# Optimization experiments

Measured on AMD Instinct MI355X. Metric: run time of the kernel, lower is better.

Reference implementation:

```python
import jax, jax.numpy as jnp
from jax import lax
import numpy as np

B, T = 32, 64
E, H, V = 512, 512, 10000


def setup_inputs() -> dict:
    key = jax.random.key(0)
    ks = jax.random.split(key, 9)
    s = 0.02
    return {
        "features": jax.random.normal(ks[0], (B, E), dtype=jnp.float32),
        "captions": jax.random.randint(ks[1], (B, T), 0, V, dtype=jnp.int64),
        "forward_approach": 0,
        "embed_table": jax.random.normal(ks[2], (V, E), dtype=jnp.float32) * s,
        "W_ih": jax.random.normal(ks[3], (4 * H, E), dtype=jnp.float32) * s,
        "W_hh": jax.random.normal(ks[4], (4 * H, H), dtype=jnp.float32) * s,
        "b_ih": jax.random.normal(ks[5], (4 * H,), dtype=jnp.float32) * s,
        "b_hh": jax.random.normal(ks[6], (4 * H,), dtype=jnp.float32) * s,
        "fc_W": jax.random.normal(ks[7], (V, H), dtype=jnp.float32) * s,
        "fc_b": jax.random.normal(ks[8], (V,), dtype=jnp.float32) * s,
    }


def reference(features, captions, forward_approach, embed_table,
              W_ih, W_hh, b_ih, b_hh, fc_W, fc_b):
    # features: [B, E]; captions: [B, T] int
    batch = features.shape[0]
    seq_len = captions.shape[1]
    hidden = W_hh.shape[1]

    # Input at step 0 is `features`; at step t>0 it is embed(captions[:, t-1]).
    emb = embed_table[captions[:, : seq_len - 1]]            # [B, T-1, E]
    xs = jnp.concatenate([features[None], jnp.transpose(emb, (1, 0, 2))],
                         axis=0)                              # [T, B, E]

    def step(carry, x):
        h, c = carry
        # PyTorch LSTMCell gate order: i, f, g, o
        gates = x @ W_ih.T + b_ih + h @ W_hh.T + b_hh         # [B, 4H]
        i, f, g, o = jnp.split(gates, 4, axis=-1)
        i = jax.nn.sigmoid(i)
        f = jax.nn.sigmoid(f)
        g = jnp.tanh(g)
        o = jax.nn.sigmoid(o)
        c = f * c + i * g
        h = o * jnp.tanh(c)
        return (h, c), h

    h0 = jnp.zeros((batch, hidden), dtype=features.dtype)
    c0 = jnp.zeros((batch, hidden), dtype=features.dtype)
    _, hs = lax.scan(step, (h0, c0), xs)                      # [T, B, H]

    logits = jnp.einsum('tbh,vh->tbv', hs, fc_W) + fc_b       # [T, B, V]
    return jnp.transpose(logits, (1, 0, 2))                   # [B, T, V]
```

## Files before the change

### kernel.cpp

```cpp
#include <hip/hip_runtime.h>
#include <hip/hip_bf16.h>

#define B_ 32
#define T_ 64
#define E_ 512
#define H_ 512
#define V_ 10000
#define G4 2048

#define NLSTM 64
#define NFC   157
#define NTOT  (NLSTM + NFC)

using bf16x8 = __attribute__((ext_vector_type(8))) short;
using f32x4  = __attribute__((ext_vector_type(4))) float;

__device__ inline f32x4 mfma16(bf16x8 a, bf16x8 b, f32x4 c) {
  return __builtin_amdgcn_mfma_f32_16x16x32_bf16(a, b, c, 0, 0, 0);
}

__device__ inline short f2bf(float x) {
  unsigned u = __builtin_bit_cast(unsigned, x);
  u = (u + 0x7fffu + ((u >> 16) & 1u)) >> 16;
  return (short)u;
}

__device__ inline float fsigm(float x) {
  return __builtin_amdgcn_rcpf(1.f + __builtin_amdgcn_exp2f(-1.442695040888963f * x));
}
__device__ inline float ftanh(float x) {
  return 1.f - 2.f * __builtin_amdgcn_rcpf(1.f + __builtin_amdgcn_exp2f(2.885390081777927f * x));
}

__device__ inline bf16x8 lds_ld16B(const short* base, int row, int col) {
  int byte = (row << 10) + (col << 1);
  byte ^= (row & 7) << 4;
  return *(const bf16x8*)((const char*)base + byte);
}

__device__ inline bf16x8 cast8(const float* src) {
  float4 f0 = *(const float4*)src;
  float4 f1 = *(const float4*)(src + 4);
  bf16x8 v;
  v[0] = f2bf(f0.x); v[1] = f2bf(f0.y); v[2] = f2bf(f0.z); v[3] = f2bf(f0.w);
  v[4] = f2bf(f1.x); v[5] = f2bf(f1.y); v[6] = f2bf(f1.z); v[7] = f2bf(f1.w);
  return v;
}


#define NW (G4 * E_)
#define NA (NW + G4)
#define NB (NA + T_ * B_ * E_)

__global__ void prep_kernel(const float* __restrict__ W_ih,
                            const float* __restrict__ b_ih, const float* __restrict__ b_hh,
                            const float* __restrict__ features, const int* __restrict__ captions,
                            const float* __restrict__ embed,
                            short* __restrict__ wih_bf, float* __restrict__ bsum,
                            short* __restrict__ xs) {
  int i = blockIdx.x * blockDim.x + threadIdx.x;
  int stride = gridDim.x * blockDim.x;
  for (; i < NB; i += stride) {
    if (i < NW) {
      wih_bf[i] = f2bf(W_ih[i]);
    } else if (i < NA) {
      int j = i - NW;
      bsum[j] = b_ih[j] + b_hh[j];
    } else {
      int j = i - NA;
      int t = j / (B_ * E_);
      int r = j - t * (B_ * E_);
      int b = r >> 9;
      int e = r & 511;
      float v;
      if (t == 0) v = features[b * E_ + e];
      else        v = embed[captions[b * T_ + (t - 1)] * E_ + e];
      xs[j] = f2bf(v);
    }
  }
}


__global__ __launch_bounds__(256) void gemm_gx_kernel(const short* __restrict__ A,
                                                      const short* __restrict__ W,
                                                      const float* __restrict__ bias,
                                                      float* __restrict__ C) {
  const int lane = threadIdx.x & 63;
  const int wv   = threadIdx.x >> 6;
  const int m0 = blockIdx.y * 64 + (wv >> 1) * 32;
  const int n0 = blockIdx.x * 64 + (wv & 1) * 32;
  const int lr = lane & 15;
  const int ko = (lane >> 4) << 3;
  f32x4 acc[2][2] = {};
  const short* Ap = A + (m0 + lr) * 512 + ko;
  const short* Wp = W + (n0 + lr) * 512 + ko;
#pragma unroll
  for (int k = 0; k < 512; k += 32) {
    bf16x8 a0 = *(const bf16x8*)(Ap + k);
    bf16x8 a1 = *(const bf16x8*)(Ap + 16 * 512 + k);
    bf16x8 b0 = *(const bf16x8*)(Wp + k);
    bf16x8 b1 = *(const bf16x8*)(Wp + 16 * 512 + k);
    acc[0][0] = mfma16(a0, b0, acc[0][0]);
    acc[0][1] = mfma16(a0, b1, acc[0][1]);
    acc[1][0] = mfma16(a1, b0, acc[1][0]);
    acc[1][1] = mfma16(a1, b1, acc[1][1]);
  }
  const int cr = (lane >> 4) * 4, cc = lane & 15;
#pragma unroll
  for (int mi = 0; mi < 2; ++mi)
#pragma unroll
    for (int ni = 0; ni < 2; ++ni)
#pragma unroll
      for (int j = 0; j < 4; ++j) {
        int row = m0 + mi * 16 + cr + j;
        int col = n0 + ni * 16 + cc;
        int tt = row >> 5, bb = row & 31;
        int g  = col >> 9, hc = col & 511;
        C[(size_t)((tt * 4 + g) * 32 + bb) * 512 + hc] = acc[mi][ni][j] + bias[col];
      }
}


__global__ __launch_bounds__(256) void fused_kernel(const float* __restrict__ WhhF,
                                                    const float* __restrict__ Gx,
                                                    short* __restrict__ hs,
                                                    int* __restrict__ flags,
                                                    const float* __restrict__ fcWF,
                                                    const float* __restrict__ fcbias,
                                                    float* __restrict__ out) {
  __shared__ short Wlds[64 * 512];
  __shared__ int tready;
  const int tid = threadIdx.x;
  int* const cnt = flags + 256;

  if (blockIdx.x < NLSTM) {
    const int blk  = blockIdx.x;
    const int bg   = blk >> 5;
    const int slot = blk & 31;
    const int hc0  = slot * 16;
    int* const gflags = flags + bg * 32;

    for (int i = tid * 8; i < 64 * 512; i += 256 * 8) {
      int gc = i >> 9;
      int k  = i & 511;
      int g  = gc >> 4, c = gc & 15;
      bf16x8 v = cast8(WhhF + (size_t)(g * 512 + hc0 + c) * 512 + k);
      int byte = (i * 2) ^ ((gc & 7) << 4);
      *(bf16x8*)((char*)Wlds + byte) = v;
    }
    __syncthreads();
    if (tid >= 64) return;

    const int lane = tid;
    const int lr  = lane & 15;
    const int ko  = (lane >> 4) << 3;
    const int cr  = (lane >> 4) << 2;
    const int cc  = lane & 15;
    const int bat = bg * 16 + cc;
    const int hrow = bg * 16 + lr;

    const float* gbase = Gx + (size_t)bat * 512 + hc0 + cr;
    float4 gx0 = *(const float4*)(gbase + 0 * 32 * 512);
    float4 gx1 = *(const float4*)(gbase + 1 * 32 * 512);
    float4 gx2 = *(const float4*)(gbase + 2 * 32 * 512);
    float4 gx3 = *(const float4*)(gbase + 3 * 32 * 512);

    float cst[4] = {0.f, 0.f, 0.f, 0.f};

    for (int t = 0; t < T_; ++t) {
      f32x4 a0 = {}, a1 = {}, a2 = {}, a3 = {};
      if (t > 0) {
        const int* fp = gflags + (lane & 31);
        for (;;) {
          int fl = __hip_atomic_load(fp, __ATOMIC_RELAXED, __HIP_MEMORY_SCOPE_AGENT);
          if (__all(fl >= t)) break;
        }
        asm volatile("" ::: "memory");
        const short* Ap = hs + (size_t)(t - 1) * (B_ * H_) + hrow * 512 + ko;
#pragma unroll
        for (int kk = 0; kk < 512; kk += 32) {
          bf16x8 hb = *(const bf16x8*)(Ap + kk);
          bf16x8 w0 = lds_ld16B(Wlds,      lr, kk + ko);
          bf16x8 w1 = lds_ld16B(Wlds, 16 + lr, kk + ko);
          bf16x8 w2 = lds_ld16B(Wlds, 32 + lr, kk + ko);
          bf16x8 w3 = lds_ld16B(Wlds, 48 + lr, kk + ko);
          a0 = mfma16(w0, hb, a0);
          a1 = mfma16(w1, hb, a1);
          a2 = mfma16(w2, hb, a2);
          a3 = mfma16(w3, hb, a3);
        }
      }
      unsigned long long hpack = 0;
#pragma unroll
      for (int j = 0; j < 4; ++j) {
        float iv = fsigm(a0[j] + ((const float*)&gx0)[j]);
        float fv = fsigm(a1[j] + ((const float*)&gx1)[j]);
        float gv = ftanh(a2[j] + ((const float*)&gx2)[j]);
        float ov = fsigm(a3[j] + ((const float*)&gx3)[j]);
        float cv = fv * cst[j] + iv * gv;
        cst[j] = cv;
        float hv = ov * ftanh(cv);
        hpack |= (unsigned long long)(unsigned short)f2bf(hv) << (16 * j);
      }
      __hip_atomic_store(
          (unsigned long long*)(hs + (size_t)t * (B_ * H_) + bat * 512 + hc0 + cr),
          hpack, __ATOMIC_RELAXED, __HIP_MEMORY_SCOPE_AGENT);
      asm volatile("s_waitcnt vmcnt(0)" ::: "memory");
      if (lane == 0) {
        if (t < T_ - 1)
          __hip_atomic_store(gflags + slot, t + 1, __ATOMIC_RELAXED,
                             __HIP_MEMORY_SCOPE_AGENT);
        __hip_atomic_fetch_add(cnt + t, 1, __ATOMIC_RELAXED,
                               __HIP_MEMORY_SCOPE_AGENT);
      }
      if (t < T_ - 1) {
        const float* g0 = gbase + (size_t)(t + 1) * 128 * 512;
        gx0 = *(const float4*)(g0 + 0 * 32 * 512);
        gx1 = *(const float4*)(g0 + 1 * 32 * 512);
        gx2 = *(const float4*)(g0 + 2 * 32 * 512);
        gx3 = *(const float4*)(g0 + 3 * 32 * 512);
      }
    }
  } else {
    const int fblk = blockIdx.x - NLSTM;
    const int n0   = fblk * 64;
    const int lane = tid & 63;
    const int wv   = tid >> 6;
    const int lr   = lane & 15;
    const int ko   = (lane >> 4) << 3;

    if (tid == 0)
      __hip_atomic_store(&tready, 0, __ATOMIC_RELAXED, __HIP_MEMORY_SCOPE_WORKGROUP);

    for (int i = tid * 8; i < 64 * 512; i += 256 * 8) {
      int gc = i >> 9;
      int k  = i & 511;
      int nr = n0 + gc; if (nr >= V_) nr = V_ - 1;
      bf16x8 v = cast8(fcWF + (size_t)nr * 512 + k);
      int byte = (i * 2) ^ ((gc & 7) << 4);
      *(bf16x8*)((char*)Wlds + byte) = v;
    }
    __syncthreads();

    const int cr = (lane >> 4) * 4, cc = lane & 15;
    const int colw = n0 + wv * 16 + cc;
    const bool wok = colw < V_;
    const float bias = wok ? fcbias[colw] : 0.f;

    for (int t = 0; t < T_; ++t) {
      if (wv == 0) {
        for (;;) {
          int c = __hip_atomic_load(cnt + t, __ATOMIC_RELAXED,
                                    __HIP_MEMORY_SCOPE_AGENT);
          if (c >= NLSTM) break;
          __builtin_amdgcn_s_sleep(32);
        }
        __hip_atomic_store(&tready, t + 1, __ATOMIC_RELAXED,
                           __HIP_MEMORY_SCOPE_WORKGROUP);
      } else {
        while (__hip_atomic_load(&tready, __ATOMIC_RELAXED,
                                 __HIP_MEMORY_SCOPE_WORKGROUP) < t + 1)
          __builtin_amdgcn_s_sleep(2);
      }
      asm volatile("" ::: "memory");
      const short* Ap = hs + (size_t)t * (B_ * H_) + lr * 512 + ko;
      f32x4 acc0 = {}, acc1 = {};
#pragma unroll
      for (int k = 0; k < 512; k += 32) {
        bf16x8 a0 = *(const bf16x8*)(Ap + k);
        bf16x8 a1 = *(const bf16x8*)(Ap + 16 * 512 + k);
        bf16x8 b  = lds_ld16B(Wlds, wv * 16 + lr, k + ko);
        acc0 = mfma16(a0, b, acc0);
        acc1 = mfma16(a1, b, acc1);
      }
      if (wok) {
#pragma unroll
        for (int j = 0; j < 4; ++j) {
          out[(size_t)(cr + j) * (T_ * V_) + t * V_ + colw]      = acc0[j] + bias;
          out[(size_t)(16 + cr + j) * (T_ * V_) + t * V_ + colw] = acc1[j] + bias;
        }
      }
    }
  }
}


extern "C" void kernel_launch(void* const* d_in, const int* in_sizes, int n_in,
                              void* d_out, int out_size, void* d_ws, size_t ws_size,
                              hipStream_t stream) {
  const float* features = (const float*)d_in[0];
  const int*   captions = (const int*)d_in[1];
  const float* embed    = (const float*)d_in[3];
  const float* W_ih     = (const float*)d_in[4];
  const float* W_hh     = (const float*)d_in[5];
  const float* b_ih     = (const float*)d_in[6];
  const float* b_hh     = (const float*)d_in[7];
  const float* fc_W     = (const float*)d_in[8];
  const float* fc_b     = (const float*)d_in[9];
  float* out = (float*)d_out;

  char* ws = (char*)d_ws;
  size_t off = 0;
  auto alloc = [&](size_t bytes) -> void* {
    off = (off + 255) & ~(size_t)255;
    void* p = ws + off;
    off += bytes;
    return p;
  };
  int*      flags  = (int*)  alloc(4096);
  short*    wih_bf = (short*)alloc((size_t)G4 * E_ * 2);
  float*    bsum   = (float*)alloc((size_t)G4 * 4);
  float*    Gx     = (float*)alloc((size_t)T_ * B_ * G4 * 4);
  short*    xs     = (short*)alloc((size_t)T_ * B_ * E_ * 2);
  short*    hs     = (short*)alloc((size_t)T_ * B_ * H_ * 2);

  (void)hipMemsetAsync(flags, 0, 4096, stream);
  prep_kernel<<<1024, 256, 0, stream>>>(W_ih, b_ih, b_hh, features, captions,
                                        embed, wih_bf, bsum, xs);
  gemm_gx_kernel<<<dim3(32, 32), 256, 0, stream>>>(xs, wih_bf, bsum, Gx);
  fused_kernel<<<NTOT, 256, 0, stream>>>(W_hh, Gx, hs, flags, fc_W, fc_b, out);
}
```

Measured before the change: 308.3 us.

## Fuse input-projection GEMM into persistent LSTM blocks using LDS-resident W_ih slices

Removes the separate gemm_gx kernel and the Gx intermediate buffer. Each LSTM block now also holds its slice of W_ih (as bf16) in shared memory and computes x_t @ W_ih^T with MFMA inside the timestep loop, before waiting on the recurrence flags. This drops a kernel launch, the W_ih conversion pass, and the Gx write and read traffic. In exchange, LDS use per block doubles to 128KB, and the extra MFMA work runs inside the serial recurrence, though it can overlap with the flag wait.

```diff
diff --git a/kernel.cpp b/kernel.cpp
--- a/kernel.cpp
+++ b/kernel.cpp
@@ -48,24 +48,17 @@
 }
 
 
-#define NW (G4 * E_)
-#define NA (NW + G4)
-#define NB (NA + T_ * B_ * E_)
-
-__global__ void prep_kernel(const float* __restrict__ W_ih,
-                            const float* __restrict__ b_ih, const float* __restrict__ b_hh,
+__global__ void prep_kernel(const float* __restrict__ b_ih, const float* __restrict__ b_hh,
                             const float* __restrict__ features, const int* __restrict__ captions,
                             const float* __restrict__ embed,
-                            short* __restrict__ wih_bf, float* __restrict__ bsum,
-                            short* __restrict__ xs) {
+                            float* __restrict__ bsum, short* __restrict__ xs) {
   int i = blockIdx.x * blockDim.x + threadIdx.x;
   int stride = gridDim.x * blockDim.x;
+  const int NA = G4;
+  const int NB = NA + T_ * B_ * E_;
   for (; i < NB; i += stride) {
-    if (i < NW) {
-      wih_bf[i] = f2bf(W_ih[i]);
-    } else if (i < NA) {
-      int j = i - NW;
-      bsum[j] = b_ih[j] + b_hh[j];
+    if (i < NA) {
+      bsum[i] = b_ih[i] + b_hh[i];
     } else {
       int j = i - NA;
       int t = j / (B_ * E_);
@@ -81,54 +74,16 @@
 }
 
 
-__global__ __launch_bounds__(256) void gemm_gx_kernel(const short* __restrict__ A,
-                                                      const short* __restrict__ W,
-                                                      const float* __restrict__ bias,
-                                                      float* __restrict__ C) {
-  const int lane = threadIdx.x & 63;
-  const int wv   = threadIdx.x >> 6;
-  const int m0 = blockIdx.y * 64 + (wv >> 1) * 32;
-  const int n0 = blockIdx.x * 64 + (wv & 1) * 32;
-  const int lr = lane & 15;
-  const int ko = (lane >> 4) << 3;
-  f32x4 acc[2][2] = {};
-  const short* Ap = A + (m0 + lr) * 512 + ko;
-  const short* Wp = W + (n0 + lr) * 512 + ko;
-#pragma unroll
-  for (int k = 0; k < 512; k += 32) {
-    bf16x8 a0 = *(const bf16x8*)(Ap + k);
-    bf16x8 a1 = *(const bf16x8*)(Ap + 16 * 512 + k);
-    bf16x8 b0 = *(const bf16x8*)(Wp + k);
-    bf16x8 b1 = *(const bf16x8*)(Wp + 16 * 512 + k);
-    acc[0][0] = mfma16(a0, b0, acc[0][0]);
-    acc[0][1] = mfma16(a0, b1, acc[0][1]);
-    acc[1][0] = mfma16(a1, b0, acc[1][0]);
-    acc[1][1] = mfma16(a1, b1, acc[1][1]);
-  }
-  const int cr = (lane >> 4) * 4, cc = lane & 15;
-#pragma unroll
-  for (int mi = 0; mi < 2; ++mi)
-#pragma unroll
-    for (int ni = 0; ni < 2; ++ni)
-#pragma unroll
-      for (int j = 0; j < 4; ++j) {
-        int row = m0 + mi * 16 + cr + j;
-        int col = n0 + ni * 16 + cc;
-        int tt = row >> 5, bb = row & 31;
-        int g  = col >> 9, hc = col & 511;
-        C[(size_t)((tt * 4 + g) * 32 + bb) * 512 + hc] = acc[mi][ni][j] + bias[col];
-      }
-}
-
-
 __global__ __launch_bounds__(256) void fused_kernel(const float* __restrict__ WhhF,
-                                                    const float* __restrict__ Gx,
+                                                    const float* __restrict__ WihF,
+                                                    const float* __restrict__ bsum,
+                                                    const short* __restrict__ xs,
                                                     short* __restrict__ hs,
                                                     int* __restrict__ flags,
                                                     const float* __restrict__ fcWF,
                                                     const float* __restrict__ fcbias,
                                                     float* __restrict__ out) {
-  __shared__ short Wlds[64 * 512];
+  __shared__ short Wlds[2 * 64 * 512];
   __shared__ int tready;
   const int tid = threadIdx.x;
   int* const cnt = flags + 256;
@@ -140,35 +95,53 @@
     const int hc0  = slot * 16;
     int* const gflags = flags + bg * 32;
 
-    for (int i = tid * 8; i < 64 * 512; i += 256 * 8) {
-      int gc = i >> 9;
-      int k  = i & 511;
+    for (int i = tid * 8; i < 2 * 64 * 512; i += 256 * 8) {
+      int region = i >> 15;
+      int local  = i & 32767;
+      int gc = local >> 9;
+      int k  = local & 511;
       int g  = gc >> 4, c = gc & 15;
-      bf16x8 v = cast8(WhhF + (size_t)(g * 512 + hc0 + c) * 512 + k);
-      int byte = (i * 2) ^ ((gc & 7) << 4);
+      const float* src = (region ? WihF : WhhF) + (size_t)(g * 512 + hc0 + c) * 512 + k;
+      bf16x8 v = cast8(src);
+      int byte = ((local * 2) ^ ((gc & 7) << 4)) + (region << 16);
       *(bf16x8*)((char*)Wlds + byte) = v;
     }
     __syncthreads();
     if (tid >= 64) return;
 
+    const short* WB = Wlds + 64 * 512;
     const int lane = tid;
     const int lr  = lane & 15;
     const int ko  = (lane >> 4) << 3;
     const int cr  = (lane >> 4) << 2;
     const int cc  = lane & 15;
     const int bat = bg * 16 + cc;
-    const int hrow = bg * 16 + lr;
-
-    const float* gbase = Gx + (size_t)bat * 512 + hc0 + cr;
-    float4 gx0 = *(const float4*)(gbase + 0 * 32 * 512);
-    float4 gx1 = *(const float4*)(gbase + 1 * 32 * 512);
-    float4 gx2 = *(const float4*)(gbase + 2 * 32 * 512);
-    float4 gx3 = *(const float4*)(gbase + 3 * 32 * 512);
+    const int brow = bg * 16 + lr;
+
+    float4 bb0 = *(const float4*)&bsum[0 * 512 + hc0 + cr];
+    float4 bb1 = *(const float4*)&bsum[1 * 512 + hc0 + cr];
+    float4 bb2 = *(const float4*)&bsum[2 * 512 + hc0 + cr];
+    float4 bb3 = *(const float4*)&bsum[3 * 512 + hc0 + cr];
 
     float cst[4] = {0.f, 0.f, 0.f, 0.f};
 
     for (int t = 0; t < T_; ++t) {
       f32x4 a0 = {}, a1 = {}, a2 = {}, a3 = {};
+      {
+        const short* Ax = xs + ((size_t)t * B_ + brow) * 512 + ko;
+#pragma unroll
+        for (int kk = 0; kk < 512; kk += 32) {
+          bf16x8 xb = *(const bf16x8*)(Ax + kk);
+          bf16x8 w0 = lds_ld16B(WB,      lr, kk + ko);
+          bf16x8 w1 = lds_ld16B(WB, 16 + lr, kk + ko);
+          bf16x8 w2 = lds_ld16B(WB, 32 + lr, kk + ko);
+          bf16x8 w3 = lds_ld16B(WB, 48 + lr, kk + ko);
+          a0 = mfma16(w0, xb, a0);
+          a1 = mfma16(w1, xb, a1);
+          a2 = mfma16(w2, xb, a2);
+          a3 = mfma16(w3, xb, a3);
+        }
+      }
       if (t > 0) {
         const int* fp = gflags + (lane & 31);
         for (;;) {
@@ -176,7 +149,7 @@
           if (__all(fl >= t)) break;
         }
         asm volatile("" ::: "memory");
-        const short* Ap = hs + (size_t)(t - 1) * (B_ * H_) + hrow * 512 + ko;
+        const short* Ap = hs + (size_t)(t - 1) * (B_ * H_) + brow * 512 + ko;
 #pragma unroll
         for (int kk = 0; kk < 512; kk += 32) {
           bf16x8 hb = *(const bf16x8*)(Ap + kk);
@@ -193,10 +166,10 @@
       unsigned long long hpack = 0;
 #pragma unroll
       for (int j = 0; j < 4; ++j) {
-        float iv = fsigm(a0[j] + ((const float*)&gx0)[j]);
-        float fv = fsigm(a1[j] + ((const float*)&gx1)[j]);
-        float gv = ftanh(a2[j] + ((const float*)&gx2)[j]);
-        float ov = fsigm(a3[j] + ((const float*)&gx3)[j]);
+        float iv = fsigm(a0[j] + ((const float*)&bb0)[j]);
+        float fv = fsigm(a1[j] + ((const float*)&bb1)[j]);
+        float gv = ftanh(a2[j] + ((const float*)&bb2)[j]);
+        float ov = fsigm(a3[j] + ((const float*)&bb3)[j]);
         float cv = fv * cst[j] + iv * gv;
         cst[j] = cv;
         float hv = ov * ftanh(cv);
@@ -212,13 +185,6 @@
                              __HIP_MEMORY_SCOPE_AGENT);
         __hip_atomic_fetch_add(cnt + t, 1, __ATOMIC_RELAXED,
                                __HIP_MEMORY_SCOPE_AGENT);
-      }
-      if (t < T_ - 1) {
-        const float* g0 = gbase + (size_t)(t + 1) * 128 * 512;
-        gx0 = *(const float4*)(g0 + 0 * 32 * 512);
-        gx1 = *(const float4*)(g0 + 1 * 32 * 512);
-        gx2 = *(const float4*)(g0 + 2 * 32 * 512);
-        gx3 = *(const float4*)(g0 + 3 * 32 * 512);
       }
     }
   } else {
@@ -307,16 +273,14 @@
     off += bytes;
     return p;
   };
-  int*      flags  = (int*)  alloc(4096);
-  short*    wih_bf = (short*)alloc((size_t)G4 * E_ * 2);
-  float*    bsum   = (float*)alloc((size_t)G4 * 4);
-  float*    Gx     = (float*)alloc((size_t)T_ * B_ * G4 * 4);
-  short*    xs     = (short*)alloc((size_t)T_ * B_ * E_ * 2);
-  short*    hs     = (short*)alloc((size_t)T_ * B_ * H_ * 2);
+  int*      flags = (int*)  alloc(4096);
+  float*    bsum  = (float*)alloc((size_t)G4 * 4);
+  short*    xs    = (short*)alloc((size_t)T_ * B_ * E_ * 2);
+  short*    hs    = (short*)alloc((size_t)T_ * B_ * H_ * 2);
 
   (void)hipMemsetAsync(flags, 0, 4096, stream);
-  prep_kernel<<<1024, 256, 0, stream>>>(W_ih, b_ih, b_hh, features, captions,
-                                        embed, wih_bf, bsum, xs);
-  gemm_gx_kernel<<<dim3(32, 32), 256, 0, stream>>>(xs, wih_bf, bsum, Gx);
-  fused_kernel<<<NTOT, 256, 0, stream>>>(W_hh, Gx, hs, flags, fc_W, fc_b, out);
-}
+  prep_kernel<<<1024, 256, 0, stream>>>(b_ih, b_hh, features, captions, embed,
+                                        bsum, xs);
+  fused_kernel<<<NTOT, 256, 0, stream>>>(W_hh, W_ih, bsum, xs, hs, flags,
+                                         fc_W, fc_b, out);
+}
```

Result: faster. 277.4 us (median of 2 runs) (-10.0%).
